# Kernel optimization log

Measured on AMD Instinct MI355X. Metric: run time of the kernel, lower is better.

The kernel has to match this reference:

```python
import jax, jax.numpy as jnp
import numpy as np

B, S, D = 2, 2048, 1024
H, DK = 16, 64          # n_heads, head dim
HI, DI = 4, 64          # indexer heads, indexer dim
TOP_K = 512
ROPE_BASE = 10000.0


def _rope(x):
    # x: [B, S, H, DK]  (torchtune-style interleaved rotary)
    half = DK // 2
    theta = 1.0 / (ROPE_BASE ** (jnp.arange(0, DK, 2, dtype=jnp.float32) / DK))  # [half]
    ang = jnp.arange(S, dtype=jnp.float32)[:, None] * theta[None, :]             # [S, half]
    cos = jnp.cos(ang)[None, :, None, :].astype(x.dtype)                          # [1,S,1,half]
    sin = jnp.sin(ang)[None, :, None, :].astype(x.dtype)
    xs = x.reshape(x.shape[:-1] + (half, 2))
    x1, x2 = xs[..., 0], xs[..., 1]
    out = jnp.stack([x1 * cos - x2 * sin, x2 * cos + x1 * sin], axis=-1)
    return out.reshape(x.shape)


def setup_inputs() -> dict:
    key = jax.random.key(0)
    ks = jax.random.split(key, 6)
    std = 0.02
    return {
        "x": jax.random.normal(ks[0], (B, S, D), dtype=jnp.float32),
        "Wqkv": jax.random.normal(ks[1], (D, 3 * D), dtype=jnp.float32) * std,
        "Wo": jax.random.normal(ks[2], (D, D), dtype=jnp.float32) * std,
        "Wq_idx": jax.random.normal(ks[3], (D, HI * DI), dtype=jnp.float32) * std,
        "Wk_idx": jax.random.normal(ks[4], (D, DI), dtype=jnp.float32) * std,
        "Ww_idx": jax.random.normal(ks[5], (D, HI), dtype=jnp.float32) * std,
    }


def reference(x, Wqkv, Wo, Wq_idx, Wk_idx, Ww_idx):
    # ---- main QKV + RoPE ----
    qkv = (x @ Wqkv).reshape(B, S, 3, H, DK)
    q, k, v = qkv[:, :, 0], qkv[:, :, 1], qkv[:, :, 2]  # [B,S,H,DK]
    q = _rope(q)
    k = _rope(k)
    Q = q.transpose(0, 2, 1, 3)  # [B,H,S,DK]
    K = k.transpose(0, 2, 1, 3)
    V = v.transpose(0, 2, 1, 3)

    # ---- lightning indexer: I[b,t,s] = sum_h w[b,t,h] * relu(q_i . k_i) ----
    qi = (x @ Wq_idx).reshape(B, S, HI, DI)
    ki = x @ Wk_idx                              # [B,S,DI]
    w = x @ Ww_idx                               # [B,S,HI]
    dots = jnp.einsum("bthd,bsd->bths", qi, ki)  # [B,S,HI,S]
    index_scores = jnp.einsum("bths,bth->bts", jax.nn.relu(dots), w)

    # ---- top-k token selection (causal penalty of -1e9, as in original) ----
    causal = jnp.triu(jnp.ones((S, S), dtype=bool), k=1)
    masked_scores = jnp.where(causal[None], -1e9, index_scores)
    _, top_idx = jax.lax.top_k(masked_scores, TOP_K)  # [B,S,TOP_K]
    b_idx = jnp.arange(B)[:, None, None]
    t_idx = jnp.arange(S)[None, :, None]
    sel_mask = jnp.zeros((B, S, S), dtype=bool).at[b_idx, t_idx, top_idx].set(True)

    # ---- masked SDPA over full S^2 (additive mask, replicating original) ----
    add_mask = jnp.where(sel_mask[:, None], 0.0, -jnp.inf).astype(Q.dtype)  # [B,1,S,S]
    logits = jnp.einsum("bhtd,bhsd->bhts", Q, K) / jnp.sqrt(jnp.float32(DK)).astype(Q.dtype)
    probs = jax.nn.softmax(logits + add_mask, axis=-1)
    attn = jnp.einsum("bhts,bhsd->bhtd", probs, V)       # [B,H,S,DK]
    attn = attn.transpose(0, 2, 1, 3).reshape(B, S, D)
    return attn @ Wo
```

## Files before the change

kernel.cpp:

```cpp
#include <hip/hip_runtime.h>
#include <hip/hip_fp16.h>
#include <hip/hip_bf16.h>
#include <math.h>

#define BB 2
#define SS 2048
#define HH 16
#define TOPK 512
#define ROWS (BB*SS)
#define KDIM 1024
#define KP 3072
#define NSTR 384

using bf16x8 = __attribute__((ext_vector_type(8))) short;
using f32x4  = __attribute__((ext_vector_type(4))) float;
typedef _Float16 f16x8 __attribute__((ext_vector_type(8)));
typedef unsigned int u32;

__device__ __forceinline__ void gload16(const void* g, void* l) {
  __builtin_amdgcn_global_load_lds(
      (const __attribute__((address_space(1))) u32*)g,
      (__attribute__((address_space(3))) u32*)l, 16, 0, 0);
}

__device__ __forceinline__ void split_bf16(float f, short& hi, short& lo) {
  __hip_bfloat16 h = __float2bfloat16(f);
  float fh = __bfloat162float(h);
  __hip_bfloat16 l = __float2bfloat16(f - fh);
  hi = *reinterpret_cast<short*>(&h);
  lo = *reinterpret_cast<short*>(&l);
}

__device__ __forceinline__ unsigned fkey(float f) {
  unsigned u = __float_as_uint(f);
  if ((u << 1) == 0u) u = 0u;
  return (u & 0x80000000u) ? ~u : (u | 0x80000000u);
}

__global__ void rope_tab_k(float* __restrict__ ct, float* __restrict__ st) {
  int idx = blockIdx.x * blockDim.x + threadIdx.x;
  if (idx >= SS * 32) return;
  int s = idx >> 5, j = idx & 31;
  float theta = 1.0f / powf(10000.0f, (float)(2 * j) / 64.0f);
  float ang = (float)s * theta;
  float sv, cv;
  sincosf(ang, &sv, &cv);
  ct[idx] = cv;
  st[idx] = sv;
}

__global__ __launch_bounds__(256) void pack_a_k(
    const float* __restrict__ X, short* __restrict__ A, int total4)
{
  int idx = blockIdx.x * 256 + threadIdx.x;
  if (idx >= total4) return;
  float4 v = ((const float4*)X)[idx];
  float a4[4] = {v.x, v.y, v.z, v.w};
  short o[12];
#pragma unroll
  for (int j = 0; j < 4; ++j) {
    short hs, ls; split_bf16(a4[j], hs, ls);
    o[3*j] = hs; o[3*j+1] = hs; o[3*j+2] = ls;
  }
  short* op = A + (size_t)idx * 12;
  *(short4*)(op)     = *(short4*)&o[0];
  *(short4*)(op + 4) = *(short4*)&o[4];
  *(short4*)(op + 8) = *(short4*)&o[8];
}

__global__ __launch_bounds__(256) void pack_bt_k(
    const float* __restrict__ W, short* __restrict__ BT, int Nw)
{
  __shared__ float tile[32][33];
  int kb = blockIdx.y * 32, nb = blockIdx.x * 32;
  int tx = threadIdx.x & 31, ty = threadIdx.x >> 5;
  for (int yy = ty; yy < 32; yy += 8) {
    float v = 0.f;
    if (nb + tx < Nw) v = W[(size_t)(kb + yy) * Nw + nb + tx];
    tile[yy][tx] = v;
  }
  __syncthreads();
  for (int yy = ty; yy < 32; yy += 8) {
    int n = nb + yy;
    if (n >= Nw) continue;
    int k = kb + tx;
    float f = tile[tx][yy];
    short hs, ls; split_bf16(f, hs, ls);
    short* orow = BT + (size_t)n * KP + 3 * k;
    orow[0] = hs; orow[1] = ls; orow[2] = hs;
  }
}

__global__ __launch_bounds__(256) void pack_wcat_k(
    const float* __restrict__ Wq, const float* __restrict__ Wk,
    const float* __restrict__ Ww, float* __restrict__ Wcat)
{
  int idx = blockIdx.x * 256 + threadIdx.x;
  if (idx >= 1024 * NSTR) return;
  int k = idx / NSTR, n = idx - k * NSTR;
  float v = 0.f;
  if (n < 256)      v = Wq[(size_t)k * 256 + n];
  else if (n < 320) v = Wk[(size_t)k * 64 + (n - 256)];
  else if (n < 324) v = Ww[(size_t)k * 4 + (n - 320)];
  Wcat[idx] = v;
}

__global__ __launch_bounds__(256) void tr_ki_k(
    const float* __restrict__ Ccat, float4* __restrict__ kiT4)
{
  int idx = blockIdx.x * 256 + threadIdx.x;
  if (idx >= BB * 16 * SS) return;
  int b = idx >> 15;
  int rem = idx & 32767;
  int d4 = rem >> 11;
  int s = rem & 2047;
  kiT4[idx] = *(const float4*)(Ccat + ((size_t)b * SS + s) * NSTR + 256 + 4 * d4);
}

__global__ __launch_bounds__(256) void gemm_bf16h(
    const short* __restrict__ A, const short* __restrict__ BT,
    __half* __restrict__ C, int M, int N, int Kp, int kLen)
{
  __shared__ short As[128 * 64];
  __shared__ short Bs[128 * 64];
  const int tid = threadIdx.x;
  const int lane = tid & 63;
  const int wv = tid >> 6;
  const int m0 = blockIdx.y * 128, n0 = blockIdx.x * 128;
  const int z = blockIdx.z;
  const int kBeg = z * kLen;
  __half* Cp = C + (size_t)z * M * N;
  const int wr = (wv >> 1) * 64, wc = (wv & 1) * 64;
  f32x4 acc[4][4];
#pragma unroll
  for (int i = 0; i < 4; ++i)
#pragma unroll
    for (int j = 0; j < 4; ++j)
#pragma unroll
      for (int r = 0; r < 4; ++r) acc[i][j][r] = 0.0f;

  const int rsel = lane & 15;
  const int lrow = lane >> 3;
  const int lcol = (lane & 7) * 8;
  for (int k0 = kBeg; k0 < kBeg + kLen; k0 += 64) {
#pragma unroll
    for (int q = 0; q < 4; ++q) {
      int c = wv * 4 + q;
      int row = c * 8 + lrow;
      gload16(A  + (size_t)(m0 + row) * Kp + k0 + lcol, &As[c * 512]);
      gload16(BT + (size_t)(n0 + row) * Kp + k0 + lcol, &Bs[c * 512]);
    }
    __syncthreads();
#pragma unroll
    for (int kk = 0; kk < 2; ++kk) {
      bf16x8 af[4], bfr[4];
      int kof = kk * 32 + (lane >> 4) * 8;
#pragma unroll
      for (int i = 0; i < 4; ++i) {
        af[i]  = *(const bf16x8*)&As[(wr + i * 16 + rsel) * 64 + kof];
        bfr[i] = *(const bf16x8*)&Bs[(wc + i * 16 + rsel) * 64 + kof];
      }
#pragma unroll
      for (int i = 0; i < 4; ++i)
#pragma unroll
        for (int j = 0; j < 4; ++j)
          acc[i][j] = __builtin_amdgcn_mfma_f32_16x16x32_bf16(af[i], bfr[j], acc[i][j], 0, 0, 0);
    }
    __syncthreads();
  }
  const int er = m0 + wr + (lane >> 4) * 4;
  const int ec = n0 + wc + rsel;
#pragma unroll
  for (int i = 0; i < 4; ++i)
#pragma unroll
    for (int j = 0; j < 4; ++j)
#pragma unroll
      for (int r = 0; r < 4; ++r)
        Cp[(size_t)(er + i * 16 + r) * N + ec + j * 16] = __float2half_rn(acc[i][j][r]);
}

__global__ __launch_bounds__(128) void gemm_idx_k(
    const float* __restrict__ A, const float* __restrict__ Bw, float* __restrict__ C)
{
  __shared__ float As[16][36];
  __shared__ float Bs[16][68];
  int n0 = blockIdx.x * 64, m0 = blockIdx.y * 32;
  int tid = threadIdx.x;
  int tr = tid >> 4;
  int tc = tid & 15;
  float acc[4][4];
#pragma unroll
  for (int i = 0; i < 4; ++i)
#pragma unroll
    for (int j = 0; j < 4; ++j) acc[i][j] = 0.f;

  for (int k0 = 0; k0 < 1024; k0 += 16) {
    {
      int lin = tid * 4;
      int row = lin >> 4, kk = lin & 15;
      float4 av = *(const float4*)(A + (size_t)(m0 + row) * 1024 + k0 + kk);
      As[kk + 0][row] = av.x; As[kk + 1][row] = av.y;
      As[kk + 2][row] = av.z; As[kk + 3][row] = av.w;
      int lin2 = tid * 8;
      int bk = lin2 >> 6, bc = lin2 & 63;
      const float* bp = Bw + (size_t)(k0 + bk) * NSTR + n0 + bc;
      *(float4*)&Bs[bk][bc]     = *(const float4*)(bp);
      *(float4*)&Bs[bk][bc + 4] = *(const float4*)(bp + 4);
    }
    __syncthreads();
#pragma unroll
    for (int k = 0; k < 16; ++k) {
      float a[4], b[4];
      *(float4*)&a[0] = *(const float4*)&As[k][tr * 4];
      *(float4*)&b[0] = *(const float4*)&Bs[k][tc * 4];
#pragma unroll
      for (int i = 0; i < 4; ++i)
#pragma unroll
        for (int j = 0; j < 4; ++j)
          acc[i][j] = fmaf(a[i], b[j], acc[i][j]);
    }
    __syncthreads();
  }
#pragma unroll
  for (int i = 0; i < 4; ++i)
    *(float4*)(C + (size_t)(m0 + tr * 4 + i) * NSTR + n0 + tc * 4) = *(float4*)&acc[i][0];
}

__global__ __launch_bounds__(256) void qkv_post_k(
    const __half* __restrict__ P, const float* __restrict__ ct, const float* __restrict__ st,
    __half* __restrict__ Qh, __half* __restrict__ Kh, __half* __restrict__ Vh)
{
  int idx = blockIdx.x * 256 + threadIdx.x;
  if (idx >= ROWS * 384) return;
  int m = idx / 384;
  int g = idx - m * 384;
  int col0 = g * 8;
  const __half* c0 = P + (size_t)m * 3072 + col0;
  const __half* c1 = c0 + (size_t)ROWS * 3072;
  float4 u = *(const float4*)c0;
  float4 v = *(const float4*)c1;
  const __half2* hu = (const __half2*)&u;
  const __half2* hv = (const __half2*)&v;
  float a[8];
#pragma unroll
  for (int c = 0; c < 4; ++c) {
    float2 x = __half22float2(hu[c]);
    float2 y = __half22float2(hv[c]);
    a[2*c]   = x.x + y.x;
    a[2*c+1] = x.y + y.y;
  }
  int sec = col0 >> 10;
  int cin = col0 & 1023;
  size_t orow = (size_t)m * 1024 + cin;
  if (sec == 2) {
    __half2 hh[4];
#pragma unroll
    for (int c = 0; c < 4; ++c) hh[c] = __floats2half2_rn(a[2*c], a[2*c+1]);
    *(float4*)(Vh + orow) = *(float4*)hh;
  } else {
    int t = m & (SS - 1);
    int jb = (cin & 63) >> 1;
    float o[8];
#pragma unroll
    for (int c = 0; c < 4; ++c) {
      float cv = ct[t * 32 + jb + c], sv = st[t * 32 + jb + c];
      float x1 = a[2*c], x2 = a[2*c+1];
      o[2*c]   = x1 * cv - x2 * sv;
      o[2*c+1] = x2 * cv + x1 * sv;
    }
    if (sec == 0) {
#pragma unroll
      for (int c = 0; c < 8; ++c) o[c] *= 0.125f;
    }
    __half2 hh[4];
#pragma unroll
    for (int c = 0; c < 4; ++c) hh[c] = __floats2half2_rn(o[2*c], o[2*c+1]);
    __half* dst = (sec == 0) ? Qh : Kh;
    *(float4*)(dst + orow) = *(float4*)hh;
  }
}

__global__ __launch_bounds__(256) void vt_k(
    const __half* __restrict__ Vh, __half* __restrict__ VhT)
{
  int st = blockIdx.x, bh = blockIdx.y;
  int b = bh >> 4, h = bh & 15;
  int s0 = st * 64;
  __shared__ __half tile[64][65];
  int tid = threadIdx.x;
#pragma unroll
  for (int rnd = 0; rnd < 2; ++rnd) {
    int row = (tid >> 3) + rnd * 32;
    int c8 = (tid & 7) * 8;
    *(float4*)&tile[row][c8] =
        *(const float4*)(Vh + ((size_t)b * SS + s0 + row) * 1024 + h * 64 + c8);
  }
  __syncthreads();
#pragma unroll
  for (int rnd = 0; rnd < 2; ++rnd) {
    int d = (tid >> 3) + rnd * 32;
    int s8 = (tid & 7) * 8;
    __half tmp[8];
#pragma unroll
    for (int j = 0; j < 8; ++j) tmp[j] = tile[s8 + j][d];
    *(float4*)(VhT + ((size_t)bh * 64 + d) * 2048 + s0 + s8) = *(float4*)tmp;
  }
}

__global__ __launch_bounds__(256) void idx_topk_k(
    const float* __restrict__ Ccat, const float4* __restrict__ kiT4,
    u32* __restrict__ msk)
{
  int b = blockIdx.y;
  int t = SS - 1 - blockIdx.x;
  int tid = threadIdx.x;
  int lane = tid & 63;
  int wv = tid >> 6;
  if (t < TOPK) {
    if (tid < 64)
      msk[((size_t)b * SS + t) * 64 + tid] = (tid < 16) ? 0xFFFFFFFFu : 0u;
    return;
  }
  __shared__ u32 uk[SS];
  __shared__ u32 hist[256];
  __shared__ u32 w[64];
  __shared__ u32 s_bsel, s_above;

  if (tid < 64) w[tid] = 0u;

  const float4* qrow = (const float4*)(Ccat + ((size_t)b * SS + t) * NSTR);
  const float* wrow = Ccat + ((size_t)b * SS + t) * NSTR + 320;
  float w0 = wrow[0], w1 = wrow[1], w2 = wrow[2], w3 = wrow[3];
  const float4* kb = kiT4 + (size_t)b * 16 * SS;

#pragma unroll 1
  for (int s0 = 0; s0 <= t; s0 += 256) {
    int s = s0 + tid;
    if (s <= t) {
      float a0 = 0.f, a1 = 0.f, a2 = 0.f, a3 = 0.f;
#pragma unroll
      for (int d4 = 0; d4 < 16; ++d4) {
        float4 kv = kb[d4 * SS + s];
        float4 q0 = qrow[d4];
        float4 q1 = qrow[16 + d4];
        float4 q2 = qrow[32 + d4];
        float4 q3 = qrow[48 + d4];
        a0 += q0.x * kv.x + q0.y * kv.y + q0.z * kv.z + q0.w * kv.w;
        a1 += q1.x * kv.x + q1.y * kv.y + q1.z * kv.z + q1.w * kv.w;
        a2 += q2.x * kv.x + q2.y * kv.y + q2.z * kv.z + q2.w * kv.w;
        a3 += q3.x * kv.x + q3.y * kv.y + q3.z * kv.z + q3.w * kv.w;
      }
      float v = fmaxf(a0, 0.f) * w0 + fmaxf(a1, 0.f) * w1 +
                fmaxf(a2, 0.f) * w2 + fmaxf(a3, 0.f) * w3;
      uk[s] = fkey(v);
    }
  }

  unsigned krem = TOPK;
  unsigned prefix = 0;
#pragma unroll 1
  for (int p = 0; p < 4; ++p) {
    int shift = 24 - 8 * p;
    u32 maskAbove = (p == 0) ? 0u : (0xFFFFFFFFu << (shift + 8));
    hist[tid] = 0u;
    __syncthreads();
#pragma unroll 1
    for (int s0 = 0; s0 <= t; s0 += 256) {
      int s = s0 + tid;
      if (s <= t) {
        u32 key = uk[s];
        if ((key & maskAbove) == prefix)
          atomicAdd(&hist[(key >> shift) & 255], 1u);
      }
    }
    __syncthreads();
    if (wv == 0) {
      uint4 hv = *(uint4*)&hist[lane * 4];
      u32 lsum = hv.x + hv.y + hv.z + hv.w;
      u32 x = lsum;
#pragma unroll
      for (int off = 1; off < 64; off <<= 1) {
        u32 y = __shfl_down(x, off);
        x += (lane + off < 64) ? y : 0u;
      }
      u32 esuf = x - lsum;
      u32 S3 = esuf + hv.w;
      u32 S2 = S3 + hv.z;
      u32 S1 = S2 + hv.y;
      u32 S0 = S1 + hv.x;
      if (S0 >= krem && S1 < krem)  { s_bsel = lane * 4 + 0; s_above = S1; }
      if (S1 >= krem && S2 < krem)  { s_bsel = lane * 4 + 1; s_above = S2; }
      if (S2 >= krem && S3 < krem)  { s_bsel = lane * 4 + 2; s_above = S3; }
      if (S3 >= krem && esuf < krem){ s_bsel = lane * 4 + 3; s_above = esuf; }
    }
    __syncthreads();
    prefix |= (s_bsel << shift);
    krem -= s_above;
  }

  u32 Tkey = prefix;
  unsigned kfin = krem;

#pragma unroll 1
  for (int s0 = 0; s0 <= t; s0 += 256) {
    int s = s0 + tid;
    bool pred = (s <= t) && (uk[s] > Tkey);
    unsigned long long mba = __ballot(pred);
    int wbase = (s0 + wv * 64) >> 5;
    if (lane == 0 && (u32)mba) atomicOr(&w[wbase], (u32)mba);
    if (lane == 32 && (u32)(mba >> 32)) atomicOr(&w[wbase + 1], (u32)(mba >> 32));
  }
  if (wv == 0) {
    unsigned taken = 0;
#pragma unroll 1
    for (int s0 = 0; s0 <= t && taken < kfin; s0 += 64) {
      int s = s0 + lane;
      bool pred = (s <= t) && (uk[s] == Tkey);
      unsigned long long mba = __ballot(pred);
      unsigned pre = (unsigned)__popcll(mba & ((1ull << lane) - 1ull));
      if (pred && (taken + pre) < kfin)
        atomicOr(&w[s >> 5], 1u << (s & 31));
      taken += (unsigned)__popcll(mba);
    }
  }
  __syncthreads();
  if (tid < 64) msk[((size_t)b * SS + t) * 64 + tid] = w[tid];
}

__global__ __launch_bounds__(256) void attn_dense_k(
    const __half* __restrict__ Qh, const __half* __restrict__ Kh,
    const __half* __restrict__ VhT, const u32* __restrict__ msk,
    short* __restrict__ Aattn)
{
  int bid = blockIdx.x;
  int xcd = bid & 7, loc = bid >> 3;
  int bh = xcd * 4 + (loc >> 5);
  int qt = 31 - (loc & 31);
  int b = bh >> 4, h = bh & 15;
  int t0 = qt * 64;
  const int ktEnd = (qt < 8) ? 7 : qt;

  const int tid = threadIdx.x;
  const int lane = tid & 63;
  const int wv = tid >> 6;
  const int l15 = lane & 15;
  const int g = lane >> 4;

  __shared__ short lds[12800];
  short* Ks = lds;
  short* Vt = lds + 4096;
  short* Ps = lds + 8192 + wv * 1088;
  u32* mlds = (u32*)(lds + 12544);

  const size_t brow = (size_t)b * SS;

  f16x8 qf0, qf1;
  {
    const __half* qp = Qh + (brow + t0 + wv * 16 + l15) * 1024 + h * 64 + g * 8;
    qf0 = *(const f16x8*)(qp);
    qf1 = *(const f16x8*)(qp + 32);
  }

  f32x4 accO[4];
#pragma unroll
  for (int n2 = 0; n2 < 4; ++n2)
#pragma unroll
    for (int r = 0; r < 4; ++r) accO[n2][r] = 0.f;
  float mRun[4] = {-1e30f, -1e30f, -1e30f, -1e30f};
  float sRun[4] = {0.f, 0.f, 0.f, 0.f};

  const int srow = lane >> 3;
  const int scp  = (lane & 7) ^ srow;

#pragma unroll 1
  for (int kt = 0; kt <= ktEnd; ++kt) {
    int kt0 = kt * 64;
#pragma unroll
    for (int q = 0; q < 2; ++q) {
      int j = wv * 2 + q;
      gload16(Kh + (brow + kt0 + j * 8 + srow) * 1024 + h * 64 + scp * 8, Ks + j * 512);
      gload16(VhT + ((size_t)(bh * 64 + j * 8 + srow)) * 2048 + kt0 + scp * 8, Vt + j * 512);
    }
    if (tid < 128)
      mlds[tid] = msk[(brow + t0 + (tid >> 1)) * 64 + kt * 2 + (tid & 1)];
    __syncthreads();

    f32x4 s4[4];
#pragma unroll
    for (int ns = 0; ns < 4; ++ns) {
#pragma unroll
      for (int r = 0; r < 4; ++r) s4[ns][r] = 0.f;
      int rowk = ns * 16 + l15;
      int cp0 = g ^ (rowk & 7);
      int cp1 = (4 + g) ^ (rowk & 7);
      f16x8 kf0 = *(const f16x8*)&Ks[rowk * 64 + cp0 * 8];
      f16x8 kf1 = *(const f16x8*)&Ks[rowk * 64 + cp1 * 8];
      s4[ns] = __builtin_amdgcn_mfma_f32_16x16x32_f16(qf0, kf0, s4[ns], 0, 0, 0);
      s4[ns] = __builtin_amdgcn_mfma_f32_16x16x32_f16(qf1, kf1, s4[ns], 0, 0, 0);
    }

#pragma unroll
    for (int r = 0; r < 4; ++r) {
      int qb2 = (wv * 16 + g * 4 + r) * 2;
      u32 w0 = mlds[qb2];
      u32 w1 = mlds[qb2 + 1];
      float le[4];
#pragma unroll
      for (int ns = 0; ns < 4; ++ns) {
        u32 w = (ns < 2) ? w0 : w1;
        int bit = (ns & 1) * 16 + l15;
        float l = s4[ns][r];
        le[ns] = ((w >> bit) & 1u) ? l : -1e30f;
      }
      float cm = fmaxf(fmaxf(le[0], le[1]), fmaxf(le[2], le[3]));
      cm = fmaxf(cm, __shfl_xor(cm, 1));
      cm = fmaxf(cm, __shfl_xor(cm, 2));
      cm = fmaxf(cm, __shfl_xor(cm, 4));
      cm = fmaxf(cm, __shfl_xor(cm, 8));
      float mn = fmaxf(mRun[r], cm);
      float fac = __expf(mRun[r] - mn);
      mRun[r] = mn;
      float sum = 0.f;
#pragma unroll
      for (int ns = 0; ns < 4; ++ns) {
        float ee = __expf(le[ns] - mn);
        ee = (le[ns] < -1e29f) ? 0.f : ee;
        sum += ee;
        Ps[(g * 4 + r) * 68 + ns * 16 + l15] =
            (short)__half_as_ushort(__float2half_rn(ee));
      }
      sum += __shfl_xor(sum, 1);
      sum += __shfl_xor(sum, 2);
      sum += __shfl_xor(sum, 4);
      sum += __shfl_xor(sum, 8);
      sRun[r] = sRun[r] * fac + sum;
#pragma unroll
      for (int n2 = 0; n2 < 4; ++n2) accO[n2][r] *= fac;
    }

    f16x8 pa0, pa1;
    {
      const short* pp = &Ps[l15 * 68 + g * 8];
      float2 lo0 = *(const float2*)(pp);
      float2 hi0 = *(const float2*)(pp + 4);
      float2 lo1 = *(const float2*)(pp + 32);
      float2 hi1 = *(const float2*)(pp + 36);
      float4 c0 = make_float4(lo0.x, lo0.y, hi0.x, hi0.y);
      float4 c1 = make_float4(lo1.x, lo1.y, hi1.x, hi1.y);
      pa0 = *(const f16x8*)&c0;
      pa1 = *(const f16x8*)&c1;
    }
#pragma unroll
    for (int n2 = 0; n2 < 4; ++n2) {
      int rowd = n2 * 16 + l15;
      int cp0 = g ^ (rowd & 7);
      int cp1 = (4 + g) ^ (rowd & 7);
      f16x8 vf0 = *(const f16x8*)&Vt[rowd * 64 + cp0 * 8];
      f16x8 vf1 = *(const f16x8*)&Vt[rowd * 64 + cp1 * 8];
      accO[n2] = __builtin_amdgcn_mfma_f32_16x16x32_f16(pa0, vf0, accO[n2], 0, 0, 0);
      accO[n2] = __builtin_amdgcn_mfma_f32_16x16x32_f16(pa1, vf1, accO[n2], 0, 0, 0);
    }
    __syncthreads();
  }

#pragma unroll
  for (int r = 0; r < 4; ++r) {
    float inv = 1.0f / sRun[r];
    size_t grow = brow + t0 + wv * 16 + g * 4 + r;
    short* arow = Aattn + grow * 3072;
#pragma unroll
    for (int n2 = 0; n2 < 4; ++n2) {
      int col = h * 64 + n2 * 16 + l15;
      float v = accO[n2][r] * inv;
      short hs, ls; split_bf16(v, hs, ls);
      short* ap = arow + 3 * col;
      ap[0] = hs; ap[1] = hs; ap[2] = ls;
    }
  }
}

__global__ __launch_bounds__(256) void redout_k(
    const __half* __restrict__ O, float* __restrict__ out)
{
  int idx = blockIdx.x * 256 + threadIdx.x;
  if (idx >= ROWS * 1024 / 8) return;
  const size_t PS = (size_t)ROWS * 1024;
  float4 u0 = *((const float4*)O + idx);
  float4 u1 = *((const float4*)(O + PS) + idx);
  float4 u2 = *((const float4*)(O + 2 * PS) + idx);
  const __half2* h0 = (const __half2*)&u0;
  const __half2* h1 = (const __half2*)&u1;
  const __half2* h2 = (const __half2*)&u2;
  float o[8];
#pragma unroll
  for (int c = 0; c < 4; ++c) {
    float2 a = __half22float2(h0[c]);
    float2 b = __half22float2(h1[c]);
    float2 d = __half22float2(h2[c]);
    o[2*c]   = a.x + b.x + d.x;
    o[2*c+1] = a.y + b.y + d.y;
  }
  float* op = out + (size_t)idx * 8;
  *(float4*)(op)     = make_float4(o[0], o[1], o[2], o[3]);
  *(float4*)(op + 4) = make_float4(o[4], o[5], o[6], o[7]);
}

extern "C" void kernel_launch(void* const* d_in, const int* in_sizes, int n_in,
                              void* d_out, int out_size, void* d_ws, size_t ws_size,
                              hipStream_t stream) {
  const float* x    = (const float*)d_in[0];
  const float* Wqkv = (const float*)d_in[1];
  const float* Wo   = (const float*)d_in[2];
  const float* Wq   = (const float*)d_in[3];
  const float* Wk   = (const float*)d_in[4];
  const float* Ww   = (const float*)d_in[5];
  float* out = (float*)d_out;

  float* fws = (float*)d_ws;
  size_t o = 0;
  __half* Qh    = (__half*)(fws + o);  o += (size_t)ROWS * 512;
  __half* Kh    = (__half*)(fws + o);  o += (size_t)ROWS * 512;
  __half* Vh    = (__half*)(fws + o);  o += (size_t)ROWS * 512;
  float*  ct    = fws + o;             o += (size_t)SS * 32;
  float*  st    = fws + o;             o += (size_t)SS * 32;
  float*  Ccat  = fws + o;             o += (size_t)ROWS * NSTR;
  short*  BTwo  = (short*)(fws + o);   o += (size_t)1024 * KP / 2;
  short*  BTq   = (short*)(fws + o);   o += (size_t)3072 * KP / 2;
  short*  Ax    = (short*)(fws + o);
  float*  Wcat  = fws + o + (size_t)ROWS * 1024;
                      o += (size_t)ROWS * KP / 2;
  __half* Ph    = (__half*)(fws + o);
  short*  Aattn = (short*)(fws + o);
  __half* VhT   = (__half*)(fws + o + (size_t)8 * 1024 * 1024);
  u32*    msk   = (u32*)(fws + o + (size_t)10500 * 1024);
  float4* kiT4  = (float4*)(fws + o + (size_t)11264 * 1024);
  o += (size_t)ROWS * 3072;
  __half* Oparts = (__half*)Qh;

  rope_tab_k<<<dim3((SS * 32 + 255) / 256), dim3(256), 0, stream>>>(ct, st);

  pack_a_k<<<dim3(ROWS * KDIM / 4 / 256), dim3(256), 0, stream>>>(x, Ax, ROWS * KDIM / 4);
  pack_bt_k<<<dim3(3072 / 32, 32), dim3(256), 0, stream>>>(Wqkv, BTq, 3072);
  pack_bt_k<<<dim3(1024 / 32, 32), dim3(256), 0, stream>>>(Wo, BTwo, 1024);

  gemm_bf16h<<<dim3(3072 / 128, ROWS / 128, 2), dim3(256), 0, stream>>>(
      Ax, BTq, Ph, ROWS, 3072, KP, KP / 2);
  qkv_post_k<<<dim3((ROWS * 384 + 255) / 256), dim3(256), 0, stream>>>(Ph, ct, st, Qh, Kh, Vh);
  vt_k<<<dim3(SS / 64, BB * HH), dim3(256), 0, stream>>>(Vh, VhT);

  pack_wcat_k<<<dim3((1024 * NSTR + 255) / 256), dim3(256), 0, stream>>>(Wq, Wk, Ww, Wcat);
  gemm_idx_k<<<dim3(NSTR / 64, ROWS / 32), dim3(128), 0, stream>>>(x, Wcat, Ccat);
  tr_ki_k<<<dim3(BB * 16 * SS / 256), dim3(256), 0, stream>>>(Ccat, kiT4);

  idx_topk_k<<<dim3(SS, BB), dim3(256), 0, stream>>>(Ccat, kiT4, msk);
  attn_dense_k<<<dim3(1024), dim3(256), 0, stream>>>(Qh, Kh, VhT, msk, Aattn);

  gemm_bf16h<<<dim3(1024 / 128, ROWS / 128, 3), dim3(256), 0, stream>>>(
      Aattn, BTwo, Oparts, ROWS, 1024, KP, KP / 3);
  redout_k<<<dim3(ROWS * 1024 / 8 / 256), dim3(256), 0, stream>>>(Oparts, out);
}
```

Before: 463.7 us.

## Fuse QKV GEMM and indexer top-k into one heterogeneous kernel launch

Merges the QKV bf16 GEMM and the indexer top-k selection into a single launch whose blocks are interleaved 3 GEMM tiles to 8 top-k rows per group. The compute-bound GEMM and the LDS/atomic-heavy top-k can then run concurrently on the same CUs. The indexer GEMM and transpose move ahead, and the workspace is rearranged so Wcat and kiT4 reuse the Qh/Kh buffers, which are only written later. The cost is a shared 32KB LDS footprint for both roles and higher register pressure from the unified kernel, which may reduce occupancy.

```diff
diff --git a/kernel.cpp b/kernel.cpp
--- a/kernel.cpp
+++ b/kernel.cpp
@@ -177,6 +177,191 @@
 #pragma unroll
       for (int r = 0; r < 4; ++r)
         Cp[(size_t)(er + i * 16 + r) * N + ec + j * 16] = __float2half_rn(acc[i][j][r]);
+}
+
+__global__ __launch_bounds__(256) void fused_qkv_topk_k(
+    const short* __restrict__ A, const short* __restrict__ BT, __half* __restrict__ C,
+    const float* __restrict__ Ccat, const float4* __restrict__ kiT4,
+    u32* __restrict__ msk)
+{
+  __shared__ char smem[32768];
+  const int tid = threadIdx.x;
+  const int lane = tid & 63;
+  const int wv = tid >> 6;
+  int bid = blockIdx.x;
+  int grp = bid / 11, off = bid - grp * 11;
+
+  if (off < 3) {
+    short* As = (short*)smem;
+    short* Bs = (short*)(smem + 16384);
+    int gb = grp * 3 + off;
+    int z = gb / 768;
+    int rem = gb - z * 768;
+    int m0 = (rem / 24) * 128;
+    int n0 = (rem % 24) * 128;
+    const int kBeg = z * (KP / 2);
+    __half* Cp = C + (size_t)z * ROWS * 3072;
+    const int wr = (wv >> 1) * 64, wc = (wv & 1) * 64;
+    f32x4 acc[4][4];
+#pragma unroll
+    for (int i = 0; i < 4; ++i)
+#pragma unroll
+      for (int j = 0; j < 4; ++j)
+#pragma unroll
+        for (int r = 0; r < 4; ++r) acc[i][j][r] = 0.0f;
+
+    const int rsel = lane & 15;
+    const int lrow = lane >> 3;
+    const int lcol = (lane & 7) * 8;
+    for (int k0 = kBeg; k0 < kBeg + KP / 2; k0 += 64) {
+#pragma unroll
+      for (int q = 0; q < 4; ++q) {
+        int c = wv * 4 + q;
+        int row = c * 8 + lrow;
+        gload16(A  + (size_t)(m0 + row) * KP + k0 + lcol, &As[c * 512]);
+        gload16(BT + (size_t)(n0 + row) * KP + k0 + lcol, &Bs[c * 512]);
+      }
+      __syncthreads();
+#pragma unroll
+      for (int kk = 0; kk < 2; ++kk) {
+        bf16x8 af[4], bfr[4];
+        int kof = kk * 32 + (lane >> 4) * 8;
+#pragma unroll
+        for (int i = 0; i < 4; ++i) {
+          af[i]  = *(const bf16x8*)&As[(wr + i * 16 + rsel) * 64 + kof];
+          bfr[i] = *(const bf16x8*)&Bs[(wc + i * 16 + rsel) * 64 + kof];
+        }
+#pragma unroll
+        for (int i = 0; i < 4; ++i)
+#pragma unroll
+          for (int j = 0; j < 4; ++j)
+            acc[i][j] = __builtin_amdgcn_mfma_f32_16x16x32_bf16(af[i], bfr[j], acc[i][j], 0, 0, 0);
+      }
+      __syncthreads();
+    }
+    const int er = m0 + wr + (lane >> 4) * 4;
+    const int ec = n0 + wc + rsel;
+#pragma unroll
+    for (int i = 0; i < 4; ++i)
+#pragma unroll
+      for (int j = 0; j < 4; ++j)
+#pragma unroll
+        for (int r = 0; r < 4; ++r)
+          Cp[(size_t)(er + i * 16 + r) * 3072 + ec + j * 16] = __float2half_rn(acc[i][j][r]);
+  } else {
+    int tb = grp * 8 + (off - 3);
+    int b = tb >> 11;
+    int t = SS - 1 - (tb & 2047);
+    if (t < TOPK) {
+      if (tid < 64)
+        msk[((size_t)b * SS + t) * 64 + tid] = (tid < 16) ? 0xFFFFFFFFu : 0u;
+      return;
+    }
+    u32* uk   = (u32*)smem;
+    u32* hist = (u32*)(smem + 8192);
+    u32* w    = (u32*)(smem + 9216);
+    u32* sv   = (u32*)(smem + 9472);
+
+    if (tid < 64) w[tid] = 0u;
+
+    const float4* qrow = (const float4*)(Ccat + ((size_t)b * SS + t) * NSTR);
+    const float* wrow = Ccat + ((size_t)b * SS + t) * NSTR + 320;
+    float w0 = wrow[0], w1 = wrow[1], w2 = wrow[2], w3 = wrow[3];
+    const float4* kb = kiT4 + (size_t)b * 16 * SS;
+
+#pragma unroll 1
+    for (int s0 = 0; s0 <= t; s0 += 256) {
+      int s = s0 + tid;
+      if (s <= t) {
+        float a0 = 0.f, a1 = 0.f, a2 = 0.f, a3 = 0.f;
+#pragma unroll
+        for (int d4 = 0; d4 < 16; ++d4) {
+          float4 kv = kb[d4 * SS + s];
+          float4 q0 = qrow[d4];
+          float4 q1 = qrow[16 + d4];
+          float4 q2 = qrow[32 + d4];
+          float4 q3 = qrow[48 + d4];
+          a0 += q0.x * kv.x + q0.y * kv.y + q0.z * kv.z + q0.w * kv.w;
+          a1 += q1.x * kv.x + q1.y * kv.y + q1.z * kv.z + q1.w * kv.w;
+          a2 += q2.x * kv.x + q2.y * kv.y + q2.z * kv.z + q2.w * kv.w;
+          a3 += q3.x * kv.x + q3.y * kv.y + q3.z * kv.z + q3.w * kv.w;
+        }
+        float v = fmaxf(a0, 0.f) * w0 + fmaxf(a1, 0.f) * w1 +
+                  fmaxf(a2, 0.f) * w2 + fmaxf(a3, 0.f) * w3;
+        uk[s] = fkey(v);
+      }
+    }
+
+    unsigned krem = TOPK;
+    unsigned prefix = 0;
+#pragma unroll 1
+    for (int p = 0; p < 4; ++p) {
+      int shift = 24 - 8 * p;
+      u32 maskAbove = (p == 0) ? 0u : (0xFFFFFFFFu << (shift + 8));
+      hist[tid] = 0u;
+      __syncthreads();
+#pragma unroll 1
+      for (int s0 = 0; s0 <= t; s0 += 256) {
+        int s = s0 + tid;
+        if (s <= t) {
+          u32 key = uk[s];
+          if ((key & maskAbove) == prefix)
+            atomicAdd(&hist[(key >> shift) & 255], 1u);
+        }
+      }
+      __syncthreads();
+      if (wv == 0) {
+        uint4 hv = *(uint4*)&hist[lane * 4];
+        u32 lsum = hv.x + hv.y + hv.z + hv.w;
+        u32 x = lsum;
+#pragma unroll
+        for (int offp = 1; offp < 64; offp <<= 1) {
+          u32 y = __shfl_down(x, offp);
+          x += (lane + offp < 64) ? y : 0u;
+        }
+        u32 esuf = x - lsum;
+        u32 S3 = esuf + hv.w;
+        u32 S2 = S3 + hv.z;
+        u32 S1 = S2 + hv.y;
+        u32 S0 = S1 + hv.x;
+        if (S0 >= krem && S1 < krem)  { sv[0] = lane * 4 + 0; sv[1] = S1; }
+        if (S1 >= krem && S2 < krem)  { sv[0] = lane * 4 + 1; sv[1] = S2; }
+        if (S2 >= krem && S3 < krem)  { sv[0] = lane * 4 + 2; sv[1] = S3; }
+        if (S3 >= krem && esuf < krem){ sv[0] = lane * 4 + 3; sv[1] = esuf; }
+      }
+      __syncthreads();
+      prefix |= (sv[0] << shift);
+      krem -= sv[1];
+    }
+
+    u32 Tkey = prefix;
+    unsigned kfin = krem;
+
+#pragma unroll 1
+    for (int s0 = 0; s0 <= t; s0 += 256) {
+      int s = s0 + tid;
+      bool pred = (s <= t) && (uk[s] > Tkey);
+      unsigned long long mba = __ballot(pred);
+      int wbase = (s0 + wv * 64) >> 5;
+      if (lane == 0 && (u32)mba) atomicOr(&w[wbase], (u32)mba);
+      if (lane == 32 && (u32)(mba >> 32)) atomicOr(&w[wbase + 1], (u32)(mba >> 32));
+    }
+    if (wv == 0) {
+      unsigned taken = 0;
+#pragma unroll 1
+      for (int s0 = 0; s0 <= t && taken < kfin; s0 += 64) {
+        int s = s0 + lane;
+        bool pred = (s <= t) && (uk[s] == Tkey);
+        unsigned long long mba = __ballot(pred);
+        unsigned pre = (unsigned)__popcll(mba & ((1ull << lane) - 1ull));
+        if (pred && (taken + pre) < kfin)
+          atomicOr(&w[s >> 5], 1u << (s & 31));
+        taken += (unsigned)__popcll(mba);
+      }
+    }
+    __syncthreads();
+    if (tid < 64) msk[((size_t)b * SS + t) * 64 + tid] = w[tid];
+  }
 }
 
 __global__ __launch_bounds__(128) void gemm_idx_k(
@@ -307,126 +492,6 @@
   }
 }
 
-__global__ __launch_bounds__(256) void idx_topk_k(
-    const float* __restrict__ Ccat, const float4* __restrict__ kiT4,
-    u32* __restrict__ msk)
-{
-  int b = blockIdx.y;
-  int t = SS - 1 - blockIdx.x;
-  int tid = threadIdx.x;
-  int lane = tid & 63;
-  int wv = tid >> 6;
-  if (t < TOPK) {
-    if (tid < 64)
-      msk[((size_t)b * SS + t) * 64 + tid] = (tid < 16) ? 0xFFFFFFFFu : 0u;
-    return;
-  }
-  __shared__ u32 uk[SS];
-  __shared__ u32 hist[256];
-  __shared__ u32 w[64];
-  __shared__ u32 s_bsel, s_above;
-
-  if (tid < 64) w[tid] = 0u;
-
-  const float4* qrow = (const float4*)(Ccat + ((size_t)b * SS + t) * NSTR);
-  const float* wrow = Ccat + ((size_t)b * SS + t) * NSTR + 320;
-  float w0 = wrow[0], w1 = wrow[1], w2 = wrow[2], w3 = wrow[3];
-  const float4* kb = kiT4 + (size_t)b * 16 * SS;
-
-#pragma unroll 1
-  for (int s0 = 0; s0 <= t; s0 += 256) {
-    int s = s0 + tid;
-    if (s <= t) {
-      float a0 = 0.f, a1 = 0.f, a2 = 0.f, a3 = 0.f;
-#pragma unroll
-      for (int d4 = 0; d4 < 16; ++d4) {
-        float4 kv = kb[d4 * SS + s];
-        float4 q0 = qrow[d4];
-        float4 q1 = qrow[16 + d4];
-        float4 q2 = qrow[32 + d4];
-        float4 q3 = qrow[48 + d4];
-        a0 += q0.x * kv.x + q0.y * kv.y + q0.z * kv.z + q0.w * kv.w;
-        a1 += q1.x * kv.x + q1.y * kv.y + q1.z * kv.z + q1.w * kv.w;
-        a2 += q2.x * kv.x + q2.y * kv.y + q2.z * kv.z + q2.w * kv.w;
-        a3 += q3.x * kv.x + q3.y * kv.y + q3.z * kv.z + q3.w * kv.w;
-      }
-      float v = fmaxf(a0, 0.f) * w0 + fmaxf(a1, 0.f) * w1 +
-                fmaxf(a2, 0.f) * w2 + fmaxf(a3, 0.f) * w3;
-      uk[s] = fkey(v);
-    }
-  }
-
-  unsigned krem = TOPK;
-  unsigned prefix = 0;
-#pragma unroll 1
-  for (int p = 0; p < 4; ++p) {
-    int shift = 24 - 8 * p;
-    u32 maskAbove = (p == 0) ? 0u : (0xFFFFFFFFu << (shift + 8));
-    hist[tid] = 0u;
-    __syncthreads();
-#pragma unroll 1
-    for (int s0 = 0; s0 <= t; s0 += 256) {
-      int s = s0 + tid;
-      if (s <= t) {
-        u32 key = uk[s];
-        if ((key & maskAbove) == prefix)
-          atomicAdd(&hist[(key >> shift) & 255], 1u);
-      }
-    }
-    __syncthreads();
-    if (wv == 0) {
-      uint4 hv = *(uint4*)&hist[lane * 4];
-      u32 lsum = hv.x + hv.y + hv.z + hv.w;
-      u32 x = lsum;
-#pragma unroll
-      for (int off = 1; off < 64; off <<= 1) {
-        u32 y = __shfl_down(x, off);
-        x += (lane + off < 64) ? y : 0u;
-      }
-      u32 esuf = x - lsum;
-      u32 S3 = esuf + hv.w;
-      u32 S2 = S3 + hv.z;
-      u32 S1 = S2 + hv.y;
-      u32 S0 = S1 + hv.x;
-      if (S0 >= krem && S1 < krem)  { s_bsel = lane * 4 + 0; s_above = S1; }
-      if (S1 >= krem && S2 < krem)  { s_bsel = lane * 4 + 1; s_above = S2; }
-      if (S2 >= krem && S3 < krem)  { s_bsel = lane * 4 + 2; s_above = S3; }
-      if (S3 >= krem && esuf < krem){ s_bsel = lane * 4 + 3; s_above = esuf; }
-    }
-    __syncthreads();
-    prefix |= (s_bsel << shift);
-    krem -= s_above;
-  }
-
-  u32 Tkey = prefix;
-  unsigned kfin = krem;
-
-#pragma unroll 1
-  for (int s0 = 0; s0 <= t; s0 += 256) {
-    int s = s0 + tid;
-    bool pred = (s <= t) && (uk[s] > Tkey);
-    unsigned long long mba = __ballot(pred);
-    int wbase = (s0 + wv * 64) >> 5;
-    if (lane == 0 && (u32)mba) atomicOr(&w[wbase], (u32)mba);
-    if (lane == 32 && (u32)(mba >> 32)) atomicOr(&w[wbase + 1], (u32)(mba >> 32));
-  }
-  if (wv == 0) {
-    unsigned taken = 0;
-#pragma unroll 1
-    for (int s0 = 0; s0 <= t && taken < kfin; s0 += 64) {
-      int s = s0 + lane;
-      bool pred = (s <= t) && (uk[s] == Tkey);
-      unsigned long long mba = __ballot(pred);
-      unsigned pre = (unsigned)__popcll(mba & ((1ull << lane) - 1ull));
-      if (pred && (taken + pre) < kfin)
-        atomicOr(&w[s >> 5], 1u << (s & 31));
-      taken += (unsigned)__popcll(mba);
-    }
-  }
-  __syncthreads();
-  if (tid < 64) msk[((size_t)b * SS + t) * 64 + tid] = w[tid];
-}
-
 __global__ __launch_bounds__(256) void attn_dense_k(
     const __half* __restrict__ Qh, const __half* __restrict__ Kh,
     const __half* __restrict__ VhT, const u32* __restrict__ msk,
@@ -626,15 +691,14 @@
   float*  Ccat  = fws + o;             o += (size_t)ROWS * NSTR;
   short*  BTwo  = (short*)(fws + o);   o += (size_t)1024 * KP / 2;
   short*  BTq   = (short*)(fws + o);   o += (size_t)3072 * KP / 2;
-  short*  Ax    = (short*)(fws + o);
-  float*  Wcat  = fws + o + (size_t)ROWS * 1024;
-                      o += (size_t)ROWS * KP / 2;
+  short*  Ax    = (short*)(fws + o);   o += (size_t)ROWS * KP / 2;
   __half* Ph    = (__half*)(fws + o);
   short*  Aattn = (short*)(fws + o);
   __half* VhT   = (__half*)(fws + o + (size_t)8 * 1024 * 1024);
-  u32*    msk   = (u32*)(fws + o + (size_t)10500 * 1024);
-  float4* kiT4  = (float4*)(fws + o + (size_t)11264 * 1024);
   o += (size_t)ROWS * 3072;
+  u32*    msk   = (u32*)(fws + o);     o += (size_t)ROWS * 64;
+  float*  Wcat  = (float*)Qh;
+  float4* kiT4  = (float4*)Kh;
   __half* Oparts = (__half*)Qh;
 
   rope_tab_k<<<dim3((SS * 32 + 255) / 256), dim3(256), 0, stream>>>(ct, st);
@@ -642,17 +706,17 @@
   pack_a_k<<<dim3(ROWS * KDIM / 4 / 256), dim3(256), 0, stream>>>(x, Ax, ROWS * KDIM / 4);
   pack_bt_k<<<dim3(3072 / 32, 32), dim3(256), 0, stream>>>(Wqkv, BTq, 3072);
   pack_bt_k<<<dim3(1024 / 32, 32), dim3(256), 0, stream>>>(Wo, BTwo, 1024);
-
-  gemm_bf16h<<<dim3(3072 / 128, ROWS / 128, 2), dim3(256), 0, stream>>>(
-      Ax, BTq, Ph, ROWS, 3072, KP, KP / 2);
+  pack_wcat_k<<<dim3((1024 * NSTR + 255) / 256), dim3(256), 0, stream>>>(Wq, Wk, Ww, Wcat);
+
+  gemm_idx_k<<<dim3(NSTR / 64, ROWS / 32), dim3(128), 0, stream>>>(x, Wcat, Ccat);
+  tr_ki_k<<<dim3(BB * 16 * SS / 256), dim3(256), 0, stream>>>(Ccat, kiT4);
+
+  fused_qkv_topk_k<<<dim3(512 * 11), dim3(256), 0, stream>>>(
+      Ax, BTq, Ph, Ccat, kiT4, msk);
+
   qkv_post_k<<<dim3((ROWS * 384 + 255) / 256), dim3(256), 0, stream>>>(Ph, ct, st, Qh, Kh, Vh);
   vt_k<<<dim3(SS / 64, BB * HH), dim3(256), 0, stream>>>(Vh, VhT);
 
-  pack_wcat_k<<<dim3((1024 * NSTR + 255) / 256), dim3(256), 0, stream>>>(Wq, Wk, Ww, Wcat);
-  gemm_idx_k<<<dim3(NSTR / 64, ROWS / 32), dim3(128), 0, stream>>>(x, Wcat, Ccat);
-  tr_ki_k<<<dim3(BB * 16 * SS / 256), dim3(256), 0, stream>>>(Ccat, kiT4);
-
-  idx_topk_k<<<dim3(SS, BB), dim3(256), 0, stream>>>(Ccat, kiT4, msk);
   attn_dense_k<<<dim3(1024), dim3(256), 0, stream>>>(Qh, Kh, VhT, msk, Aattn);
 
   gemm_bf16h<<<dim3(1024 / 128, ROWS / 128, 3), dim3(256), 0, stream>>>(
```

Result: slower. 519.1 us (+11.9%).
